# Kernel tuning notes

Measured on AMD Instinct MI355X. Metric: run time of the kernel, lower is better.

## Reference

```python
import jax, jax.numpy as jnp
import numpy as np

DIM = 768
HEADS = 12
HEAD_DIM = DIM // HEADS
HIDDEN = int(DIM * 4.0)


def setup_inputs() -> dict:
    key = jax.random.key(0)
    ks = jax.random.split(key, 12)
    s = lambda *shape: 0.02
    inp = {
        "x": jax.random.normal(ks[0], (8, 1024, DIM), dtype=jnp.float32),
        "norm1_g": jnp.ones((DIM,), jnp.float32),
        "norm1_b": jnp.zeros((DIM,), jnp.float32),
        "qkv_w": jax.random.normal(ks[1], (DIM, 3 * DIM), jnp.float32) * 0.02,
        "qkv_b": jnp.zeros((3 * DIM,), jnp.float32),
        "proj_w": jax.random.normal(ks[2], (DIM, DIM), jnp.float32) * 0.02,
        "proj_b": jnp.zeros((DIM,), jnp.float32),
        "norm2_g": jnp.ones((DIM,), jnp.float32),
        "norm2_b": jnp.zeros((DIM,), jnp.float32),
        "fc1_w": jax.random.normal(ks[3], (DIM, HIDDEN), jnp.float32) * 0.02,
        "fc1_b": jnp.zeros((HIDDEN,), jnp.float32),
        "fc2_w": jax.random.normal(ks[4], (HIDDEN, DIM), jnp.float32) * 0.02,
        "fc2_b": jnp.zeros((DIM,), jnp.float32),
    }
    return inp


def _layernorm(x, g, b, eps=1e-5):
    mu = jnp.mean(x, axis=-1, keepdims=True)
    var = jnp.mean(jnp.square(x - mu), axis=-1, keepdims=True)
    return (x - mu) * jax.lax.rsqrt(var + eps) * g + b


def _attention(x, qkv_w, qkv_b, proj_w, proj_b):
    B, N, C = x.shape
    qkv = x @ qkv_w + qkv_b                      # [B, N, 3C]
    qkv = qkv.reshape(B, N, 3, HEADS, HEAD_DIM)
    q, k, v = jnp.moveaxis(qkv, 2, 0)            # each [B, N, H, D]
    scale = HEAD_DIM ** -0.5
    scores = jnp.einsum("bnhd,bmhd->bhnm", q, k) * scale  # [B, H, N, N]
    attn = jax.nn.softmax(scores, axis=-1)
    out = jnp.einsum("bhnm,bmhd->bnhd", attn, v).reshape(B, N, C)
    return out @ proj_w + proj_b


def reference(x, norm1_g, norm1_b, qkv_w, qkv_b, proj_w, proj_b,
              norm2_g, norm2_b, fc1_w, fc1_b, fc2_w, fc2_b):
    # Pre-norm transformer block (inference: DropPath = identity)
    x = x + _attention(_layernorm(x, norm1_g, norm1_b), qkv_w, qkv_b, proj_w, proj_b)
    h = _layernorm(x, norm2_g, norm2_b)
    h = jax.nn.gelu(h @ fc1_w + fc1_b, approximate=False) @ fc2_w + fc2_b
    return x + h
```

## Files before the change

### kernel.cpp

```cpp
#include <hip/hip_runtime.h>

typedef __attribute__((ext_vector_type(8))) short s16x8;
typedef __attribute__((ext_vector_type(4))) short s16x4;
typedef __attribute__((ext_vector_type(4))) float f32x4;

static __device__ __forceinline__ short f2bf(float f) {
    unsigned u = __builtin_bit_cast(unsigned, f);
    u = (u + 0x7FFFu + ((u >> 16) & 1u)) >> 16;
    return (short)u;
}

__device__ __forceinline__ void gload16(const short* g, short* l) {
    __builtin_amdgcn_global_load_lds(
        (const __attribute__((address_space(1))) void*)g,
        (__attribute__((address_space(3))) void*)l,
        16, 0, 0);
}

__global__ __launch_bounds__(256) void transpose_convert(
    const float* __restrict__ W, short* __restrict__ Wt, int K, int N)
{
    __shared__ float tile[32][33];
    const int bx = blockIdx.x * 32;
    const int by = blockIdx.y * 32;
    const int tx = threadIdx.x;
    const int ty = threadIdx.y;
    for (int i = 0; i < 32; i += 8)
        tile[ty + i][tx] = W[(size_t)(by + ty + i) * N + bx + tx];
    __syncthreads();
    for (int i = 0; i < 32; i += 8)
        Wt[(size_t)(bx + ty + i) * K + by + tx] = f2bf(tile[tx][ty + i]);
}

__global__ __launch_bounds__(256) void layernorm_kernel(
    const float* __restrict__ x, const float* __restrict__ g,
    const float* __restrict__ b, short* __restrict__ out)
{
    const int row = blockIdx.x;
    const float* xr = x + (size_t)row * 768;
    const int t = threadIdx.x;
    float v0 = xr[t], v1 = xr[t + 256], v2 = xr[t + 512];
    __shared__ float red[4];

    float s = v0 + v1 + v2;
    for (int off = 32; off >= 1; off >>= 1) s += __shfl_down(s, off, 64);
    if ((t & 63) == 0) red[t >> 6] = s;
    __syncthreads();
    const float mean = (red[0] + red[1] + red[2] + red[3]) * (1.0f / 768.0f);
    const float d0 = v0 - mean, d1 = v1 - mean, d2 = v2 - mean;
    __syncthreads();
    float ss = d0 * d0 + d1 * d1 + d2 * d2;
    for (int off = 32; off >= 1; off >>= 1) ss += __shfl_down(ss, off, 64);
    if ((t & 63) == 0) red[t >> 6] = ss;
    __syncthreads();
    const float var = (red[0] + red[1] + red[2] + red[3]) * (1.0f / 768.0f);
    const float rstd = rsqrtf(var + 1e-5f);
    out[(size_t)row * 768 + t]       = f2bf(d0 * rstd * g[t] + b[t]);
    out[(size_t)row * 768 + t + 256] = f2bf(d1 * rstd * g[t + 256] + b[t + 256]);
    out[(size_t)row * 768 + t + 512] = f2bf(d2 * rstd * g[t + 512] + b[t + 512]);
}

#define G128_STAGE(AS, BS)                                                  \
    {                                                                       \
        _Pragma("unroll") for (int c = 0; c < 4; c++) {                     \
            gload16(aP[c], &AS[(w * 4 + c) * 512]); aP[c] += 64;            \
            gload16(bP[c], &BS[(w * 4 + c) * 512]); bP[c] += 64;            \
        }                                                                   \
    }

#define G128_COMPUTE(AS, BS)                                                \
    {                                                                       \
        s16x8 af[4][2], bf[4][2];                                           \
        _Pragma("unroll") for (int m = 0; m < 4; m++) {                     \
            const int rbase = (wr + m * 16 + fr) * 64;                      \
            af[m][0] = *(const s16x8*)&AS[rbase + ((g ^ sl) * 8)];          \
            af[m][1] = *(const s16x8*)&AS[rbase + (((4 + g) ^ sl) * 8)];    \
        }                                                                   \
        _Pragma("unroll") for (int n = 0; n < 4; n++) {                     \
            const int rbase = (wc + n * 16 + fr) * 64;                      \
            bf[n][0] = *(const s16x8*)&BS[rbase + ((g ^ sl) * 8)];          \
            bf[n][1] = *(const s16x8*)&BS[rbase + (((4 + g) ^ sl) * 8)];    \
        }                                                                   \
        _Pragma("unroll") for (int m = 0; m < 4; m++)                       \
            _Pragma("unroll") for (int n = 0; n < 4; n++) {                 \
                acc[m][n] = __builtin_amdgcn_mfma_f32_16x16x32_bf16(af[m][0], bf[n][0], acc[m][n], 0, 0, 0); \
                acc[m][n] = __builtin_amdgcn_mfma_f32_16x16x32_bf16(af[m][1], bf[n][1], acc[m][n], 0, 0, 0); \
            }                                                               \
    }

template <int MODE>
__global__ __launch_bounds__(256) void gemm_db128(
    const short* __restrict__ A, const short* __restrict__ Bt,
    const float* __restrict__ bias, void* __restrict__ out,
    short* __restrict__ vtout, int M, int N, int K)
{
    __shared__ __align__(16) short As0[128 * 64];
    __shared__ __align__(16) short As1[128 * 64];
    __shared__ __align__(16) short Bs0[128 * 64];
    __shared__ __align__(16) short Bs1[128 * 64];

    const int t = threadIdx.x;
    const int l = t & 63;
    const int w = t >> 6;
    const int wr = (w >> 1) * 64;
    const int wc = (w & 1) * 64;

    const int ncol = N >> 7;
    const int xcd = blockIdx.x & 7;
    const int idx = blockIdx.x >> 3;
    const int tn = (idx % ncol) << 7;
    const int tm = ((idx / ncol) * 8 + xcd) << 7;

    const int srow = l >> 3;
    const int scol = ((l & 7) ^ srow) * 8;
    const short* aP[4]; const short* bP[4];
#pragma unroll
    for (int c = 0; c < 4; c++) {
        aP[c] = A  + (size_t)(tm + (w * 4 + c) * 8 + srow) * K + scol;
        bP[c] = Bt + (size_t)(tn + (w * 4 + c) * 8 + srow) * K + scol;
    }

    const int fr = l & 15;
    const int g = l >> 4;
    const int sl = fr & 7;

    f32x4 acc[4][4] = {};

    G128_STAGE(As0, Bs0);
    __syncthreads();

    const int half = K >> 7;
    for (int it = 0; it < half; ++it) {
        G128_STAGE(As1, Bs1);
        G128_COMPUTE(As0, Bs0);
        __syncthreads();
        if (it < half - 1) G128_STAGE(As0, Bs0);
        G128_COMPUTE(As1, Bs1);
        __syncthreads();
    }

    const int fq = g * 4;
#pragma unroll
    for (int m = 0; m < 4; m++) {
#pragma unroll
        for (int n = 0; n < 4; n++) {
            const int col = tn + wc + n * 16 + fr;
            const float bv = bias[col];
            if (MODE == 3 && col >= 1536) {
                const int row0 = tm + wr + m * 16 + fq;
                const int bb = row0 >> 10;
                const int nseq = row0 & 1023;
                s16x4 ov;
#pragma unroll
                for (int j = 0; j < 4; j++) ov[j] = f2bf(acc[m][n][j] + bv);
                *(s16x4*)(vtout + (((size_t)(bb * 768 + (col - 1536))) << 10) + nseq) = ov;
            } else {
#pragma unroll
                for (int j = 0; j < 4; j++) {
                    const int row = tm + wr + m * 16 + fq + j;
                    float v = acc[m][n][j] + bv;
                    if (MODE == 2) {
                        const float u = v * (0.7978845608f + 0.0356774081f * v * v);
                        const float e = __builtin_amdgcn_exp2f(u * 2.8853900817779268f);
                        v = v - v * __builtin_amdgcn_rcpf(e + 1.0f);
                    }
                    ((short*)out)[(size_t)row * N + col] = f2bf(v);
                }
            }
        }
    }
}

#define G_STAGE(AS, BS)                                                     \
    {                                                                       \
        _Pragma("unroll") for (int c = 0; c < 4; c++) {                     \
            gload16(aP[c], &AS[(w * 4 + c) * 512]); aP[c] += 64;            \
        }                                                                   \
        _Pragma("unroll") for (int c = 0; c < 2; c++) {                     \
            gload16(bP[c], &BS[(w * 2 + c) * 512]); bP[c] += 64;            \
        }                                                                   \
    }

#define G_COMPUTE(AS, BS)                                                   \
    {                                                                       \
        s16x8 af[4][2], bf[2][2];                                           \
        _Pragma("unroll") for (int m = 0; m < 4; m++) {                     \
            const int rbase = (wr + m * 16 + fr) * 64;                      \
            af[m][0] = *(const s16x8*)&AS[rbase + ((g ^ sl) * 8)];          \
            af[m][1] = *(const s16x8*)&AS[rbase + (((4 + g) ^ sl) * 8)];    \
        }                                                                   \
        _Pragma("unroll") for (int n = 0; n < 2; n++) {                     \
            const int rbase = (wc + n * 16 + fr) * 64;                      \
            bf[n][0] = *(const s16x8*)&BS[rbase + ((g ^ sl) * 8)];          \
            bf[n][1] = *(const s16x8*)&BS[rbase + (((4 + g) ^ sl) * 8)];    \
        }                                                                   \
        _Pragma("unroll") for (int m = 0; m < 4; m++)                       \
            _Pragma("unroll") for (int n = 0; n < 2; n++) {                 \
                acc[m][n] = __builtin_amdgcn_mfma_f32_16x16x32_bf16(af[m][0], bf[n][0], acc[m][n], 0, 0, 0); \
                acc[m][n] = __builtin_amdgcn_mfma_f32_16x16x32_bf16(af[m][1], bf[n][1], acc[m][n], 0, 0, 0); \
            }                                                               \
    }

__global__ __launch_bounds__(256) void gemm_bt_db(
    const short* __restrict__ A, const short* __restrict__ Bt,
    const float* __restrict__ bias, const float* __restrict__ res,
    float* __restrict__ out, int M, int N, int K)
{
    __shared__ __align__(16) short As0[128 * 64];
    __shared__ __align__(16) short As1[128 * 64];
    __shared__ __align__(16) short Bs0[64 * 64];
    __shared__ __align__(16) short Bs1[64 * 64];

    const int t = threadIdx.x;
    const int l = t & 63;
    const int w = t >> 6;
    const int wr = (w >> 1) * 64;
    const int wc = (w & 1) * 32;

    const int ncol = N >> 6;
    const int xcd = blockIdx.x & 7;
    const int idx = blockIdx.x >> 3;
    const int tn = (idx % ncol) << 6;
    const int tm = ((idx / ncol) * 8 + xcd) << 7;

    const int srow = l >> 3;
    const int scol = ((l & 7) ^ srow) * 8;
    const short* aP[4]; const short* bP[2];
#pragma unroll
    for (int c = 0; c < 4; c++)
        aP[c] = A  + (size_t)(tm + (w * 4 + c) * 8 + srow) * K + scol;
#pragma unroll
    for (int c = 0; c < 2; c++)
        bP[c] = Bt + (size_t)(tn + (w * 2 + c) * 8 + srow) * K + scol;

    const int fr = l & 15;
    const int g = l >> 4;
    const int sl = fr & 7;

    f32x4 acc[4][2] = {};

    G_STAGE(As0, Bs0);
    __syncthreads();

    const int half = K >> 7;
    for (int it = 0; it < half; ++it) {
        G_STAGE(As1, Bs1);
        G_COMPUTE(As0, Bs0);
        __syncthreads();
        if (it < half - 1) G_STAGE(As0, Bs0);
        G_COMPUTE(As1, Bs1);
        __syncthreads();
    }

    const int fq = g * 4;
#pragma unroll
    for (int m = 0; m < 4; m++) {
#pragma unroll
        for (int n = 0; n < 2; n++) {
            const int col = tn + wc + n * 16 + fr;
            const float bv = bias[col];
#pragma unroll
            for (int j = 0; j < 4; j++) {
                const int row = tm + wr + m * 16 + fq + j;
                out[(size_t)row * N + col] = acc[m][n][j] + bv + res[(size_t)row * N + col];
            }
        }
    }
}

#define ATTN_STAGE(KS, VS)                                                  \
    {                                                                       \
        gload16(kP,                    &KS[w * 1024]);                      \
        gload16(kP + (size_t)8 * 2304, &KS[w * 1024 + 512]);                \
        gload16(vP,                    &VS[w * 1024]);                      \
        gload16(vP + (size_t)8 * 1024, &VS[w * 1024 + 512]);                \
        kP += (size_t)64 * 2304;                                            \
        vP += 64;                                                           \
    }

#define ATTN_COMPUTE(KS, VS)                                                \
    {                                                                       \
        s16x8 ka[4][2];                                                     \
        _Pragma("unroll") for (int n = 0; n < 4; n++) {                     \
            const int rbase = (n * 16 + lq) * 64;                           \
            ka[n][0] = *(const s16x8*)&KS[rbase + ((g * 8) ^ swz)];         \
            ka[n][1] = *(const s16x8*)&KS[rbase + ((32 + g * 8) ^ swz)];    \
        }                                                                   \
        f32x4 s[2][4];                                                      \
        _Pragma("unroll") for (int r = 0; r < 2; r++)                       \
            _Pragma("unroll") for (int n = 0; n < 4; n++) {                 \
                f32x4 sv = {};                                              \
                sv = __builtin_amdgcn_mfma_f32_16x16x32_bf16(ka[n][0], qb[r][0], sv, 0, 0, 0); \
                sv = __builtin_amdgcn_mfma_f32_16x16x32_bf16(ka[n][1], qb[r][1], sv, 0, 0, 0); \
                s[r][n] = sv;                                               \
            }                                                               \
        s16x8 va[4][2];                                                     \
        _Pragma("unroll") for (int dt = 0; dt < 4; dt++) {                  \
            const int rbase = (dt * 16 + lq) * 64;                          \
            va[dt][0] = *(const s16x8*)&VS[rbase + ((g * 8) ^ swz)];        \
            va[dt][1] = *(const s16x8*)&VS[rbase + ((32 + g * 8) ^ swz)];   \
        }                                                                   \
        _Pragma("unroll") for (int r = 0; r < 2; r++) {                     \
            float mx = fmaxf(fmaxf(s[r][0][0], s[r][0][1]), fmaxf(s[r][0][2], s[r][0][3])); \
            _Pragma("unroll") for (int n = 1; n < 4; n++)                   \
                mx = fmaxf(mx, fmaxf(fmaxf(s[r][n][0], s[r][n][1]), fmaxf(s[r][n][2], s[r][n][3]))); \
            const float mxs = mx * kSc;                                     \
            if (!__all(mxs - m_run[r] <= 8.0f)) {                           \
                float gm = mxs;                                             \
                gm = fmaxf(gm, __shfl_xor(gm, 16, 64));                     \
                gm = fmaxf(gm, __shfl_xor(gm, 32, 64));                     \
                const float mnew = fmaxf(m_run[r], gm);                     \
                const float alpha = __builtin_amdgcn_exp2f(m_run[r] - mnew);\
                m_run[r] = mnew;                                            \
                l_run[r] *= alpha;                                          \
                _Pragma("unroll") for (int dt = 0; dt < 4; dt++) {          \
                    acc[r][dt][0] *= alpha; acc[r][dt][1] *= alpha;         \
                    acc[r][dt][2] *= alpha; acc[r][dt][3] *= alpha;         \
                }                                                           \
            }                                                               \
            const float mb = m_run[r];                                      \
            float ssum = 0.f;                                               \
            _Pragma("unroll") for (int n = 0; n < 4; n++) {                 \
                const float p0 = __builtin_amdgcn_exp2f(s[r][n][0] * kSc - mb); \
                const float p1 = __builtin_amdgcn_exp2f(s[r][n][1] * kSc - mb); \
                const float p2 = __builtin_amdgcn_exp2f(s[r][n][2] * kSc - mb); \
                const float p3 = __builtin_amdgcn_exp2f(s[r][n][3] * kSc - mb); \
                ssum += (p0 + p1) + (p2 + p3);                              \
                unsigned lo, hi;                                            \
                asm("v_cvt_pk_bf16_f32 %0, %1, %2" : "=v"(lo) : "v"(p0), "v"(p1)); \
                asm("v_cvt_pk_bf16_f32 %0, %1, %2" : "=v"(hi) : "v"(p2), "v"(p3)); \
                unsigned* pp = (unsigned*)&Ps[w][r * 16 + lq][n * 16 + g * 4]; \
                pp[0] = lo; pp[1] = hi;                                     \
            }                                                               \
            l_run[r] += ssum;                                               \
        }                                                                   \
        _Pragma("unroll") for (int r = 0; r < 2; r++) {                     \
            const s16x8 pb0 = *(const s16x8*)&Ps[w][r * 16 + lq][g * 8];    \
            const s16x8 pb1 = *(const s16x8*)&Ps[w][r * 16 + lq][32 + g * 8]; \
            _Pragma("unroll") for (int dt = 0; dt < 4; dt++) {              \
                acc[r][dt] = __builtin_amdgcn_mfma_f32_16x16x32_bf16(va[dt][0], pb0, acc[r][dt], 0, 0, 0); \
                acc[r][dt] = __builtin_amdgcn_mfma_f32_16x16x32_bf16(va[dt][1], pb1, acc[r][dt], 0, 0, 0); \
            }                                                               \
        }                                                                   \
    }

__global__ __launch_bounds__(256) void attn_kernel(
    const short* __restrict__ qkv, const short* __restrict__ vTg,
    short* __restrict__ out)
{
    const int bid = blockIdx.x;
    const int x = bid & 7;
    const int i = bid >> 3;
    const int bh = x + 8 * (i % 12);
    const int qt = i / 12;
    const int b = bh / 12, h = bh % 12;

    __shared__ __align__(16) short Ks0[64 * 64];
    __shared__ __align__(16) short Ks1[64 * 64];
    __shared__ __align__(16) short Vs0[64 * 64];
    __shared__ __align__(16) short Vs1[64 * 64];
    __shared__ __align__(16) short Ps[4][32][72];

    const int t = threadIdx.x;
    const int l = t & 63;
    const int w = t >> 6;
    const int lq = l & 15;
    const int g = l >> 4;
    const float kSc = 0.18033688011112042f;

    const int q0 = b * 1024 + qt * 128 + w * 32;

    s16x8 qb[2][2];
#pragma unroll
    for (int r = 0; r < 2; r++) {
        const short* qp = qkv + ((size_t)(q0 + r * 16 + lq)) * 2304 + h * 64 + g * 8;
        qb[r][0] = *(const s16x8*)qp;
        qb[r][1] = *(const s16x8*)(qp + 32);
    }

    const int srow = l >> 3;
    const int scol = ((l & 7) ^ srow) * 8;
    const short* kP = qkv + (size_t)(b * 1024 + w * 16 + srow) * 2304 + 768 + h * 64 + scol;
    const short* vP = vTg + (size_t)(bh * 64 + w * 16 + srow) * 1024 + scol;

    f32x4 acc[2][4] = {};
    float m_run[2] = {-1e30f, -1e30f};
    float l_run[2] = {0.f, 0.f};

    const int swz = (lq & 7) * 8;

    ATTN_STAGE(Ks0, Vs0);
    __syncthreads();

    for (int it = 0; it < 8; ++it) {
        ATTN_STAGE(Ks1, Vs1);
        ATTN_COMPUTE(Ks0, Vs0);
        __syncthreads();
        if (it < 7) ATTN_STAGE(Ks0, Vs0);
        ATTN_COMPUTE(Ks1, Vs1);
        __syncthreads();
    }

#pragma unroll
    for (int r = 0; r < 2; r++) {
        float ls = l_run[r];
        ls += __shfl_xor(ls, 16, 64);
        ls += __shfl_xor(ls, 32, 64);
        const float rinv = 1.0f / ls;
        const int qrow = q0 + r * 16 + lq;
#pragma unroll
        for (int dt = 0; dt < 4; dt++) {
            s16x4 ov;
#pragma unroll
            for (int j = 0; j < 4; j++) ov[j] = f2bf(acc[r][dt][j] * rinv);
            *(s16x4*)(out + (size_t)qrow * 768 + h * 64 + dt * 16 + g * 4) = ov;
        }
    }
}

extern "C" void kernel_launch(void* const* d_in, const int* in_sizes, int n_in,
                              void* d_out, int out_size, void* d_ws, size_t ws_size,
                              hipStream_t stream) {
    const float* x      = (const float*)d_in[0];
    const float* n1g    = (const float*)d_in[1];
    const float* n1b    = (const float*)d_in[2];
    const float* qkv_w  = (const float*)d_in[3];
    const float* qkv_b  = (const float*)d_in[4];
    const float* proj_w = (const float*)d_in[5];
    const float* proj_b = (const float*)d_in[6];
    const float* n2g    = (const float*)d_in[7];
    const float* n2b    = (const float*)d_in[8];
    const float* fc1_w  = (const float*)d_in[9];
    const float* fc1_b  = (const float*)d_in[10];
    const float* fc2_w  = (const float*)d_in[11];
    const float* fc2_b  = (const float*)d_in[12];
    float* out = (float*)d_out;

    char* ws = (char*)d_ws;
    short* qkv_wT  = (short*)(ws + 0);
    short* proj_wT = (short*)(ws + 3538944);
    short* fc1_wT  = (short*)(ws + 4718592);
    short* fc2_wT  = (short*)(ws + 9437184);
    short* bufA    = (short*)(ws + 14155776);
    short* bufB    = (short*)(ws + 26738688);
    short* vT      = (short*)(ws + 64487424);
    float* bufC    = (float*)(ws + 77070336);

    const dim3 tb(32, 8);
    transpose_convert<<<dim3(2304 / 32, 768 / 32), tb, 0, stream>>>(qkv_w, qkv_wT, 768, 2304);
    transpose_convert<<<dim3(768 / 32, 768 / 32),  tb, 0, stream>>>(proj_w, proj_wT, 768, 768);
    transpose_convert<<<dim3(3072 / 32, 768 / 32), tb, 0, stream>>>(fc1_w, fc1_wT, 768, 3072);
    transpose_convert<<<dim3(768 / 32, 3072 / 32), tb, 0, stream>>>(fc2_w, fc2_wT, 3072, 768);

    layernorm_kernel<<<8192, 256, 0, stream>>>(x, n1g, n1b, bufA);

    gemm_db128<3><<<64 * (2304 / 128), 256, 0, stream>>>(
        bufA, qkv_wT, qkv_b, bufB, vT, 8192, 2304, 768);

    attn_kernel<<<768, 256, 0, stream>>>(bufB, vT, bufA);

    gemm_bt_db<<<64 * (768 / 64), 256, 0, stream>>>(
        bufA, proj_wT, proj_b, x, bufC, 8192, 768, 768);

    layernorm_kernel<<<8192, 256, 0, stream>>>(bufC, n2g, n2b, bufA);

    gemm_db128<2><<<64 * (3072 / 128), 256, 0, stream>>>(
        bufA, fc1_wT, fc1_b, bufB, nullptr, 8192, 3072, 768);

    gemm_bt_db<<<64 * (768 / 64), 256, 0, stream>>>(
        bufB, fc2_wT, fc2_b, bufC, out, 8192, 768, 3072);
}
```

Before: 251.8 us.

## Use 256x128 tiles with a three-stage LDS pipeline in the QKV and FC1 GEMMs

The double-buffered 128x128 GEMM used for QKV and FC1 becomes a 512-thread kernel with 256x128 tiles and a three-buffer LDS ring. Explicit `vmcnt(6)` waits plus raw barriers keep one stage of global-to-LDS loads in flight while the current stage is computed. The aim is to hide global load latency better and to reuse each B tile across more rows. In exchange it uses about 144KB of LDS per block, so only one block fits per CU. The loop is hardcoded for K=768 (12 k-steps), so other K values would give wrong results.

Result: no change. 253.3 us (+0.6%).

```diff
diff --git a/kernel.cpp b/kernel.cpp
--- a/kernel.cpp
+++ b/kernel.cpp
@@ -60,26 +60,28 @@
     out[(size_t)row * 768 + t + 512] = f2bf(d2 * rstd * g[t + 512] + b[t + 512]);
 }
 
-#define G128_STAGE(AS, BS)                                                  \
+#define P_STAGE(ASB, BSB)                                                   \
     {                                                                       \
         _Pragma("unroll") for (int c = 0; c < 4; c++) {                     \
-            gload16(aP[c], &AS[(w * 4 + c) * 512]); aP[c] += 64;            \
-            gload16(bP[c], &BS[(w * 4 + c) * 512]); bP[c] += 64;            \
-        }                                                                   \
-    }
-
-#define G128_COMPUTE(AS, BS)                                                \
+            gload16(aP[c], &ASB[(w * 4 + c) * 512]); aP[c] += 64;           \
+        }                                                                   \
+        _Pragma("unroll") for (int c = 0; c < 2; c++) {                     \
+            gload16(bP[c], &BSB[(w * 2 + c) * 512]); bP[c] += 64;           \
+        }                                                                   \
+    }
+
+#define P_COMPUTE(ASB, BSB)                                                 \
     {                                                                       \
         s16x8 af[4][2], bf[4][2];                                           \
         _Pragma("unroll") for (int m = 0; m < 4; m++) {                     \
-            const int rbase = (wr + m * 16 + fr) * 64;                      \
-            af[m][0] = *(const s16x8*)&AS[rbase + ((g ^ sl) * 8)];          \
-            af[m][1] = *(const s16x8*)&AS[rbase + (((4 + g) ^ sl) * 8)];    \
+            const int rb = (wr + m * 16 + fr) * 64;                         \
+            af[m][0] = *(const s16x8*)&ASB[rb + ((g ^ sl) * 8)];            \
+            af[m][1] = *(const s16x8*)&ASB[rb + (((4 + g) ^ sl) * 8)];      \
         }                                                                   \
         _Pragma("unroll") for (int n = 0; n < 4; n++) {                     \
-            const int rbase = (wc + n * 16 + fr) * 64;                      \
-            bf[n][0] = *(const s16x8*)&BS[rbase + ((g ^ sl) * 8)];          \
-            bf[n][1] = *(const s16x8*)&BS[rbase + (((4 + g) ^ sl) * 8)];    \
+            const int rb = (wc + n * 16 + fr) * 64;                         \
+            bf[n][0] = *(const s16x8*)&BSB[rb + ((g ^ sl) * 8)];            \
+            bf[n][1] = *(const s16x8*)&BSB[rb + (((4 + g) ^ sl) * 8)];      \
         }                                                                   \
         _Pragma("unroll") for (int m = 0; m < 4; m++)                       \
             _Pragma("unroll") for (int n = 0; n < 4; n++) {                 \
@@ -88,16 +90,28 @@
             }                                                               \
     }
 
+#define P_SYNC6                                                             \
+    asm volatile("s_waitcnt vmcnt(6)" ::: "memory");                        \
+    __builtin_amdgcn_s_barrier();                                           \
+    __builtin_amdgcn_sched_barrier(0);
+
+#define P_SYNC0                                                             \
+    asm volatile("s_waitcnt vmcnt(0)" ::: "memory");                        \
+    __builtin_amdgcn_s_barrier();                                           \
+    __builtin_amdgcn_sched_barrier(0);
+
 template <int MODE>
-__global__ __launch_bounds__(256) void gemm_db128(
+__global__ __launch_bounds__(512) void gemm_pipe3(
     const short* __restrict__ A, const short* __restrict__ Bt,
     const float* __restrict__ bias, void* __restrict__ out,
     short* __restrict__ vtout, int M, int N, int K)
 {
-    __shared__ __align__(16) short As0[128 * 64];
-    __shared__ __align__(16) short As1[128 * 64];
+    __shared__ __align__(16) short As0[256 * 64];
+    __shared__ __align__(16) short As1[256 * 64];
+    __shared__ __align__(16) short As2[256 * 64];
     __shared__ __align__(16) short Bs0[128 * 64];
     __shared__ __align__(16) short Bs1[128 * 64];
+    __shared__ __align__(16) short Bs2[128 * 64];
 
     const int t = threadIdx.x;
     const int l = t & 63;
@@ -109,16 +123,17 @@
     const int xcd = blockIdx.x & 7;
     const int idx = blockIdx.x >> 3;
     const int tn = (idx % ncol) << 7;
-    const int tm = ((idx / ncol) * 8 + xcd) << 7;
+    const int tm = ((idx / ncol) * 8 + xcd) << 8;
 
     const int srow = l >> 3;
     const int scol = ((l & 7) ^ srow) * 8;
-    const short* aP[4]; const short* bP[4];
-#pragma unroll
-    for (int c = 0; c < 4; c++) {
+    const short* aP[4]; const short* bP[2];
+#pragma unroll
+    for (int c = 0; c < 4; c++)
         aP[c] = A  + (size_t)(tm + (w * 4 + c) * 8 + srow) * K + scol;
-        bP[c] = Bt + (size_t)(tn + (w * 4 + c) * 8 + srow) * K + scol;
-    }
+#pragma unroll
+    for (int c = 0; c < 2; c++)
+        bP[c] = Bt + (size_t)(tn + (w * 2 + c) * 8 + srow) * K + scol;
 
     const int fr = l & 15;
     const int g = l >> 4;
@@ -126,18 +141,19 @@
 
     f32x4 acc[4][4] = {};
 
-    G128_STAGE(As0, Bs0);
-    __syncthreads();
-
-    const int half = K >> 7;
-    for (int it = 0; it < half; ++it) {
-        G128_STAGE(As1, Bs1);
-        G128_COMPUTE(As0, Bs0);
-        __syncthreads();
-        if (it < half - 1) G128_STAGE(As0, Bs0);
-        G128_COMPUTE(As1, Bs1);
-        __syncthreads();
-    }
+    P_STAGE(As0, Bs0);
+    P_STAGE(As1, Bs1);
+    P_SYNC6;
+
+#pragma unroll 1
+    for (int i = 0; i < 3; ++i) {
+        P_STAGE(As2, Bs2); P_COMPUTE(As0, Bs0); P_SYNC6;
+        P_STAGE(As0, Bs0); P_COMPUTE(As1, Bs1); P_SYNC6;
+        P_STAGE(As1, Bs1); P_COMPUTE(As2, Bs2); P_SYNC6;
+    }
+    P_STAGE(As2, Bs2); P_COMPUTE(As0, Bs0); P_SYNC6;
+    P_COMPUTE(As1, Bs1); P_SYNC0;
+    P_COMPUTE(As2, Bs2);
 
     const int fq = g * 4;
 #pragma unroll
@@ -454,7 +470,7 @@
 
     layernorm_kernel<<<8192, 256, 0, stream>>>(x, n1g, n1b, bufA);
 
-    gemm_db128<3><<<64 * (2304 / 128), 256, 0, stream>>>(
+    gemm_pipe3<3><<<(8192 / 256) * (2304 / 128), 512, 0, stream>>>(
         bufA, qkv_wT, qkv_b, bufB, vT, 8192, 2304, 768);
 
     attn_kernel<<<768, 256, 0, stream>>>(bufB, vT, bufA);
@@ -464,7 +480,7 @@
 
     layernorm_kernel<<<8192, 256, 0, stream>>>(bufC, n2g, n2b, bufA);
 
-    gemm_db128<2><<<64 * (3072 / 128), 256, 0, stream>>>(
+    gemm_pipe3<2><<<(8192 / 256) * (3072 / 128), 512, 0, stream>>>(
         bufA, fc1_wT, fc1_b, bufB, nullptr, 8192, 3072, 768);
 
     gemm_bt_db<<<64 * (768 / 64), 256, 0, stream>>>(
```
